# Kernel optimization log

Measured on AMD Instinct MI355X. Metric: run time of the kernel, lower is better.

Reference implementation:

```python
import jax, jax.numpy as jnp
import numpy as np

DIM = 768

def setup_inputs() -> dict:
    key = jax.random.key(0)
    k1, k2, k3, k4, k5 = jax.random.split(key, 5)
    B, S, D = 16, 1024, DIM
    x = jax.random.normal(k1, (B, S, D), dtype=jnp.float32)
    # torch Linear weights: W has shape [out, in], y = x @ W.T + b
    w_qkv = jax.random.normal(k2, (3 * D, D), dtype=jnp.float32) * (D ** -0.5)
    b_qkv = jax.random.normal(k3, (3 * D,), dtype=jnp.float32) * 0.01
    w_out = jax.random.normal(k4, (D, D), dtype=jnp.float32) * (D ** -0.5)
    b_out = jax.random.normal(k5, (D,), dtype=jnp.float32) * 0.01
    return {"x": x, "w_qkv": w_qkv, "b_qkv": b_qkv, "w_out": w_out, "b_out": b_out}

def reference(x, w_qkv, b_qkv, w_out, b_out):
    D = x.shape[-1]
    qkv = jnp.einsum('bsd,ed->bse', x, w_qkv) + b_qkv  # [B,S,3D]
    q, k, v = jnp.split(qkv, 3, axis=-1)
    scale = D ** -0.5
    att = jnp.einsum('bqd,bkd->bqk', q, k) * scale  # [B,S,S]
    att = jax.nn.softmax(att, axis=-1)
    # dropout (p=0.1) is identity in eval mode
    out = jnp.einsum('bqk,bkd->bqd', att, v)
    return jnp.einsum('bsd,ed->bse', out, w_out) + b_out
```

## Files before the change

kernel.cpp:

```cpp
#include <hip/hip_runtime.h>
#include <hip/hip_bf16.h>
#include <math.h>

typedef __attribute__((ext_vector_type(8))) short bf16x8;
typedef __attribute__((ext_vector_type(4))) float f32x4;

#define SCALE_QK 0.03608439182435162f

__device__ __forceinline__ unsigned short f2bf_rne(float f) {
    union { float f; unsigned u; } x; x.f = f;
    unsigned r = x.u + 0x7FFFu + ((x.u >> 16) & 1u);
    return (unsigned short)(r >> 16);
}

__device__ __forceinline__ void store4(unsigned short* p, float v0, float v1, float v2, float v3) {
    ushort4 o; o.x = f2bf_rne(v0); o.y = f2bf_rne(v1); o.z = f2bf_rne(v2); o.w = f2bf_rne(v3);
    *(ushort4*)p = o;
}
__device__ __forceinline__ void store4(float* p, float v0, float v1, float v2, float v3) {
    float4 o; o.x = v0; o.y = v1; o.z = v2; o.w = v3;
    *(float4*)p = o;
}

__device__ __forceinline__ void async_copy16(const void* g, void* l) {
    __builtin_amdgcn_global_load_lds(
        (const __attribute__((address_space(1))) void*)g,
        (__attribute__((address_space(3))) void*)l, 16, 0, 0);
}

__device__ __forceinline__ void gemm_core128(
    unsigned short* shA, unsigned short* shB,
    const unsigned short* __restrict__ A, int lda,
    const unsigned short* __restrict__ B, int ldb,
    long long tileM, long long tileN, int K,
    int t, int wm, int wn, int quad, int l16, f32x4 (&acc)[4][4])
{
    for (int k0 = 0; k0 < K; k0 += 64) {
        __syncthreads();
#pragma unroll
        for (int p = 0; p < 4; ++p) {
            const int g   = p * 256 + t;
            const int row = g >> 3;
            const int kg  = (g & 7) ^ (row & 7);
            async_copy16(A + (tileM + row) * (long long)lda + k0 + kg * 8, &shA[g << 3]);
            async_copy16(B + (tileN + row) * (long long)ldb + k0 + kg * 8, &shB[g << 3]);
        }
        __syncthreads();

#pragma unroll 1
        for (int h = 0; h < 2; ++h) {
            bf16x8 af[4], bfr[4];
#pragma unroll
            for (int mi = 0; mi < 4; ++mi) {
                const int row = wm + mi * 16 + l16;
                const int kg  = ((h << 2) | quad) ^ (row & 7);
                af[mi] = *(const bf16x8*)(&shA[row * 64 + kg * 8]);
            }
#pragma unroll
            for (int ni = 0; ni < 4; ++ni) {
                const int row = wn + ni * 16 + l16;
                const int kg  = ((h << 2) | quad) ^ (row & 7);
                bfr[ni] = *(const bf16x8*)(&shB[row * 64 + kg * 8]);
            }
#pragma unroll
            for (int mi = 0; mi < 4; ++mi)
#pragma unroll
                for (int ni = 0; ni < 4; ++ni)
                    acc[mi][ni] = __builtin_amdgcn_mfma_f32_16x16x32_bf16(
                        bfr[ni], af[mi], acc[mi][ni], 0, 0, 0);
        }
    }
}

__global__ __launch_bounds__(256) void prep(
    const float* __restrict__ w_qkv, const float* __restrict__ b_qkv,
    const float* __restrict__ w_out, const float* __restrict__ b_out,
    unsigned short* __restrict__ wqT, unsigned short* __restrict__ wkT,
    unsigned short* __restrict__ wvT, unsigned short* __restrict__ wob,
    float* __restrict__ v2f, float* __restrict__ bpp)
{
    const int blk = blockIdx.x;
    const int t   = threadIdx.x;
    if (blk < 432) {
        __shared__ float sh[64][65];
        const int m  = blk / 144;
        const int r  = blk % 144;
        const int ty = r / 12;
        const int tx = r % 12;
        const float* W = w_qkv + (long long)m * 768 * 768;
        unsigned short* WT = (m == 0) ? wqT : (m == 1) ? wkT : wvT;
        const int il = t & 63;
        const int ob = t >> 6;
#pragma unroll
        for (int it = 0; it < 16; ++it) {
            const int ol = ob + it * 4;
            sh[ol][il] = W[(long long)(ty * 64 + ol) * 768 + tx * 64 + il];
        }
        __syncthreads();
#pragma unroll
        for (int it = 0; it < 16; ++it) {
            const int il2 = ob + it * 4;
            WT[(long long)(tx * 64 + il2) * 768 + ty * 64 + il] = f2bf_rne(sh[il][il2]);
        }
    } else if (blk < 624) {
        const int d = (blk - 432) * 4 + (t >> 6);
        const int l = t & 63;
        float s = 0.f;
        for (int o = l; o < 768; o += 64)
            s += w_out[(long long)d * 768 + o] * b_qkv[1536 + o];
        for (int off = 1; off < 64; off <<= 1) s += __shfl_xor(s, off);
        if (l == 0) bpp[d] = b_out[d] + s;
    } else if (blk < 636) {
        __shared__ float pvv[4][64];
        const int i0   = (blk - 624) * 64;
        const int il   = t & 63;
        const int wave = t >> 6;
        const float* Wk = w_qkv + 768LL * 768;
        float a = 0.f;
        for (int o = wave * 192; o < wave * 192 + 192; ++o)
            a += Wk[(long long)o * 768 + i0 + il] * b_qkv[o];
        pvv[wave][il] = a;
        __syncthreads();
        if (t < 64) v2f[i0 + t] = pvv[0][t] + pvv[1][t] + pvv[2][t] + pvv[3][t];
    } else {
        const int j = (blk - 636) * 256 + t;
        float4 v = ((const float4*)w_out)[j];
        ushort4 o;
        o.x = f2bf_rne(v.x); o.y = f2bf_rne(v.y);
        o.z = f2bf_rne(v.z); o.w = f2bf_rne(v.w);
        ((ushort4*)wob)[j] = o;
    }
}

__global__ __launch_bounds__(256) void wgemm_cvt(
    const unsigned short* __restrict__ wkT, const unsigned short* __restrict__ wqT,
    const unsigned short* __restrict__ wob, const unsigned short* __restrict__ wvT,
    unsigned short* __restrict__ B2,
    const float* __restrict__ x, unsigned short* __restrict__ xb,
    const float* __restrict__ v2f, float* __restrict__ wf)
{
    const int t = threadIdx.x;
    if (blockIdx.x < 72) {
        __shared__ unsigned short shA[8192];
        __shared__ unsigned short shB[8192];
        const int lane = t & 63;
        const int wave = t >> 6;
        const int wm   = (wave & 1) * 64;
        const int wn   = (wave >> 1) * 64;
        const int quad = lane >> 4;
        const int l16  = lane & 15;
        const int z  = blockIdx.x / 36;
        const int r  = blockIdx.x % 36;
        const long long tileM = (long long)(r / 6) * 128;
        const long long tileN = (long long)(r % 6) * 128;
        const unsigned short* A  = z ? wob : wkT;
        const unsigned short* Bp = z ? wvT : wqT;
        unsigned short* C = B2 + (long long)z * 768 * 768;
        const float sc = z ? 1.0f : SCALE_QK;

        f32x4 acc[4][4];
#pragma unroll
        for (int i = 0; i < 4; ++i)
#pragma unroll
            for (int j = 0; j < 4; ++j)
#pragma unroll
                for (int rr = 0; rr < 4; ++rr) acc[i][j][rr] = 0.0f;

        gemm_core128(shA, shB, A, 768, Bp, 768, tileM, tileN, 768,
                     t, wm, wn, quad, l16, acc);

#pragma unroll
        for (int mi = 0; mi < 4; ++mi) {
            const long long gm = tileM + wm + mi * 16 + l16;
#pragma unroll
            for (int ni = 0; ni < 4; ++ni) {
                const long long gn0 = tileN + wn + ni * 16 + quad * 4;
                const f32x4 a = acc[mi][ni];
                store4(C + gm * 768 + gn0, a[0] * sc, a[1] * sc, a[2] * sc, a[3] * sc);
            }
        }
    } else {
        const int wave = t >> 6;
        const int lane = t & 63;
        const long long row = (long long)(blockIdx.x - 72) * 4 + wave;
        const float4* xr = (const float4*)x + row * 192;
        ushort4* xbr = (ushort4*)xb + row * 192;
        const float4* v2 = (const float4*)v2f;
        float w = 0.f;
#pragma unroll
        for (int j = 0; j < 3; ++j) {
            const int c = j * 64 + lane;
            float4 v = xr[c];
            ushort4 o;
            o.x = f2bf_rne(v.x); o.y = f2bf_rne(v.y);
            o.z = f2bf_rne(v.z); o.w = f2bf_rne(v.w);
            xbr[c] = o;
            float4 b = v2[c];
            w += v.x * b.x + v.y * b.y + v.z * b.z + v.w * b.w;
        }
#pragma unroll
        for (int off = 1; off < 64; off <<= 1) w += __shfl_xor(w, off);
        if (lane == 0) wf[row] = w * SCALE_QK;
    }
}

template <typename OutT, bool DO_EXP, bool DO_RSCALE, bool DO_VT>
__global__ __launch_bounds__(256) void gemm_nt_bf16(
    const unsigned short* __restrict__ A, int lda, long long strideA,
    const unsigned short* __restrict__ B, int ldb, long long strideB,
    OutT* __restrict__ C, int ldc, long long strideC,
    const float* __restrict__ bias, float scale, int K,
    float* __restrict__ rowsum, const float* __restrict__ rscale,
    unsigned short* __restrict__ vtp, const float* __restrict__ wf)
{
    __shared__ unsigned short shA[DO_VT ? 8448 : 8192];
    __shared__ unsigned short shB[DO_VT ? 8448 : 8192];

    const int t    = threadIdx.x;
    const int lane = t & 63;
    const int wave = t >> 6;
    const int wm   = (wave & 1) * 64;
    const int wn   = (wave >> 1) * 64;
    const int quad = lane >> 4;
    const int l16  = lane & 15;

    const int gx = gridDim.x, gy = gridDim.y;
    const int nwg = gx * gy * gridDim.z;
    const int orig = blockIdx.x + gx * (blockIdx.y + gy * blockIdx.z);
    const int id  = (orig & 7) * (nwg >> 3) + (orig >> 3);
    const int bx  = id % gx;
    const int rem = id / gx;
    const int by  = rem % gy;
    const int bz  = rem / gy;

    const long long batch = bz;
    A += batch * strideA;
    B += batch * strideB;
    C += batch * strideC;

    const long long tileM = (long long)by * 128;
    const long long tileN = (long long)bx * 128;
    const long long rowsPerBatch = (long long)gy * 128;

    f32x4 acc[4][4];
#pragma unroll
    for (int i = 0; i < 4; ++i)
#pragma unroll
        for (int j = 0; j < 4; ++j)
#pragma unroll
            for (int r = 0; r < 4; ++r) acc[i][j][r] = 0.0f;

    gemm_core128(shA, shB, A, lda, B, ldb, tileM, tileN, K, t, wm, wn, quad, l16, acc);

    const bool vt_block = DO_VT && (tileN >= 768) && (tileN < 1536);
    if (vt_block) __syncthreads();
    unsigned short* const shd = (wn == 0) ? shA : shB;

    float wkv[4][4];
    if (DO_EXP) {
        const float* wfb = wf + batch * rowsPerBatch;
#pragma unroll
        for (int ni = 0; ni < 4; ++ni) {
            const long long gn0 = tileN + wn + ni * 16 + quad * 4;
            float4 t4 = *(const float4*)&wfb[gn0];
            wkv[ni][0] = t4.x; wkv[ni][1] = t4.y; wkv[ni][2] = t4.z; wkv[ni][3] = t4.w;
        }
    }
#pragma unroll
    for (int mi = 0; mi < 4; ++mi) {
        const long long gm = tileM + wm + mi * 16 + l16;
        float w = scale;
        if (DO_RSCALE) {
            float s = 0.f;
#pragma unroll
            for (int j = 0; j < 16; ++j)
                s += rscale[((long long)j * gridDim.z + batch) * rowsPerBatch + gm];
            w = scale / s;
        }
        float rsum = 0.0f;
#pragma unroll
        for (int ni = 0; ni < 4; ++ni) {
            const long long gn0 = tileN + wn + ni * 16 + quad * 4;
            float b0 = 0.f, b1 = 0.f, b2 = 0.f, b3 = 0.f;
            if (bias) {
                float4 bv = *(const float4*)&bias[gn0];
                b0 = bv.x; b1 = bv.y; b2 = bv.z; b3 = bv.w;
            }
            const f32x4 a = acc[mi][ni];
            float v0, v1, v2, v3;
            if (DO_EXP) {
                v0 = __expf(a[0] + wkv[ni][0]);
                v1 = __expf(a[1] + wkv[ni][1]);
                v2 = __expf(a[2] + wkv[ni][2]);
                v3 = __expf(a[3] + wkv[ni][3]);
                rsum += (v0 + v1) + (v2 + v3);
            } else {
                v0 = a[0] * w + b0; v1 = a[1] * w + b1;
                v2 = a[2] * w + b2; v3 = a[3] * w + b3;
            }
            if (vt_block) {
                const int dl = ni * 16 + quad * 4;
                const int kl = wm + mi * 16 + l16;
                shd[(dl + 0) * 132 + kl] = f2bf_rne(v0);
                shd[(dl + 1) * 132 + kl] = f2bf_rne(v1);
                shd[(dl + 2) * 132 + kl] = f2bf_rne(v2);
                shd[(dl + 3) * 132 + kl] = f2bf_rne(v3);
            } else {
                store4(C + gm * (long long)ldc + gn0, v0, v1, v2, v3);
            }
        }
        if (DO_EXP) {
            rsum += __shfl_xor(rsum, 16);
            rsum += __shfl_xor(rsum, 32);
            if (quad == 0) {
                const long long slot = (long long)(bx * 2 + (wn >> 6));
                rowsum[(slot * gridDim.z + batch) * rowsPerBatch + gm] = rsum;
            }
        }
    }
    if (vt_block) {
        __syncthreads();
        const long long bvt  = tileM >> 10;
        const long long kin0 = tileM & 1023;
        const int dr = t >> 1;
        const int hf = t & 1;
        const unsigned short* src = (dr < 64) ? &shA[dr * 132] : &shB[(dr - 64) * 132];
        unsigned short* dst = vtp + (bvt * 768 + (tileN - 768) + dr) * 1024 + kin0 + hf * 64;
        src += hf * 64;
#pragma unroll
        for (int j = 0; j < 16; ++j)
            *(uint2*)(dst + j * 4) = *(const uint2*)(src + j * 4);
    }
}

extern "C" void kernel_launch(void* const* d_in, const int* in_sizes, int n_in,
                              void* d_out, int out_size, void* d_ws, size_t ws_size,
                              hipStream_t stream) {
    (void)in_sizes; (void)n_in; (void)out_size; (void)ws_size;

    const float* x     = (const float*)d_in[0];
    const float* w_qkv = (const float*)d_in[1];
    const float* b_qkv = (const float*)d_in[2];
    const float* w_out = (const float*)d_in[3];
    const float* b_out = (const float*)d_in[4];
    float* out = (float*)d_out;

    const int B = 16, S = 1024, D = 768;
    const long long MS = (long long)B * S;
    const int NB2 = 1536;

    unsigned short* xb  = (unsigned short*)d_ws;
    unsigned short* wob = xb  + MS * D;
    unsigned short* wqT = wob + (long long)D * D;
    unsigned short* wkT = wqT + (long long)D * D;
    unsigned short* wvT = wkT + (long long)D * D;
    unsigned short* B2  = wvT + (long long)D * D;
    unsigned short* xm  = B2  + (long long)NB2 * D;
    unsigned short* vwt = xm  + MS * D;
    unsigned short* att = vwt + (long long)B * D * S;
    float* rpart = (float*)(att + (long long)B * S * S);
    float* v2f   = rpart + 16 * MS;
    float* bpp   = v2f + D;
    float* wf    = bpp + D;

    prep<<<1212, 256, 0, stream>>>(w_qkv, b_qkv, w_out, b_out,
                                   wqT, wkT, wvT, wob, v2f, bpp);

    wgemm_cvt<<<4168, 256, 0, stream>>>(wkT, wqT, wob, wvT, B2, x, xb, v2f, wf);

    gemm_nt_bf16<unsigned short, false, false, true><<<dim3(NB2 / 128, (int)(MS / 128), 1), 256, 0, stream>>>(
        xb, D, 0, B2, D, 0, xm, D, 0, nullptr, 1.0f, D, nullptr, nullptr, vwt, nullptr);

    gemm_nt_bf16<unsigned short, true, false, false><<<dim3(S / 128, S / 128, B), 256, 0, stream>>>(
        xm, D, (long long)S * D,
        xb, D, (long long)S * D,
        att, S, (long long)S * S, nullptr, 1.0f, D, rpart, nullptr, nullptr, wf);

    gemm_nt_bf16<float, false, true, false><<<dim3(D / 128, S / 128, B), 256, 0, stream>>>(
        att, S, (long long)S * S,
        vwt, S, (long long)D * S,
        out, D, (long long)S * D, bpp, 1.0f, S, nullptr, rpart, nullptr, nullptr);
}
```

Measured before the change: 262.7 us.

## Add dedicated 128x256-tile attention score kernel with fused exp and rowsum

Splits the QK^T exp stage out of the generic GEMM template into its own kernel with a 128x256 output tile per workgroup (each wave computes 64x128). This halves the number of row-sum partial slots from 16 to 8 and raises reuse of the A tile, cutting global loads per output. The larger per-wave accumulator (32 MFMA tiles) raises register pressure and may lower occupancy. The loop also loads directly without the shared gemm_core pipeline, so it may lose any double buffering that core had.

```diff
diff --git a/kernel.cpp b/kernel.cpp
--- a/kernel.cpp
+++ b/kernel.cpp
@@ -204,14 +204,126 @@
     }
 }
 
-template <typename OutT, bool DO_EXP, bool DO_RSCALE, bool DO_VT>
+__global__ __launch_bounds__(256) void attn(
+    const unsigned short* __restrict__ A, long long strideA,
+    const unsigned short* __restrict__ B, long long strideB,
+    unsigned short* __restrict__ C, long long strideC,
+    const float* __restrict__ wf, float* __restrict__ rpart)
+{
+    __shared__ unsigned short shA[128 * 64];
+    __shared__ unsigned short shB[256 * 64];
+
+    const int t    = threadIdx.x;
+    const int lane = t & 63;
+    const int wave = t >> 6;
+    const int wm   = (wave & 1) * 64;
+    const int wk   = (wave >> 1);
+    const int quad = lane >> 4;
+    const int l16  = lane & 15;
+
+    const int nwg  = 512;
+    const int orig = blockIdx.x + 4 * (blockIdx.y + 8 * blockIdx.z);
+    const int id   = (orig & 7) * (nwg >> 3) + (orig >> 3);
+    const int bx   = id & 3;
+    const int rem  = id >> 2;
+    const int by   = rem & 7;
+    const int bz   = rem >> 3;
+
+    const long long batch = bz;
+    A += batch * strideA;
+    B += batch * strideB;
+    C += batch * strideC;
+    const long long tileM = (long long)by * 128;
+    const long long tileN = (long long)bx * 256;
+
+    f32x4 acc[4][8];
+#pragma unroll
+    for (int i = 0; i < 4; ++i)
+#pragma unroll
+        for (int j = 0; j < 8; ++j)
+#pragma unroll
+            for (int r = 0; r < 4; ++r) acc[i][j][r] = 0.0f;
+
+    for (int k0 = 0; k0 < 768; k0 += 64) {
+        __syncthreads();
+#pragma unroll
+        for (int p = 0; p < 4; ++p) {
+            const int g   = p * 256 + t;
+            const int row = g >> 3;
+            const int kg  = (g & 7) ^ (row & 7);
+            async_copy16(A + (tileM + row) * 768LL + k0 + kg * 8, &shA[g << 3]);
+        }
+#pragma unroll
+        for (int p = 0; p < 8; ++p) {
+            const int g   = p * 256 + t;
+            const int row = g >> 3;
+            const int kg  = (g & 7) ^ (row & 7);
+            async_copy16(B + (tileN + row) * 768LL + k0 + kg * 8, &shB[g << 3]);
+        }
+        __syncthreads();
+
+#pragma unroll 1
+        for (int h = 0; h < 2; ++h) {
+            bf16x8 af[4], bfr[8];
+#pragma unroll
+            for (int mi = 0; mi < 4; ++mi) {
+                const int row = wm + mi * 16 + l16;
+                const int kg  = ((h << 2) | quad) ^ (row & 7);
+                af[mi] = *(const bf16x8*)(&shA[row * 64 + kg * 8]);
+            }
+#pragma unroll
+            for (int ni = 0; ni < 8; ++ni) {
+                const int row = wk * 128 + ni * 16 + l16;
+                const int kg  = ((h << 2) | quad) ^ (row & 7);
+                bfr[ni] = *(const bf16x8*)(&shB[row * 64 + kg * 8]);
+            }
+#pragma unroll
+            for (int mi = 0; mi < 4; ++mi)
+#pragma unroll
+                for (int ni = 0; ni < 8; ++ni)
+                    acc[mi][ni] = __builtin_amdgcn_mfma_f32_16x16x32_bf16(
+                        bfr[ni], af[mi], acc[mi][ni], 0, 0, 0);
+        }
+    }
+
+    float wkv[8][4];
+#pragma unroll
+    for (int ni = 0; ni < 8; ++ni) {
+        const long long gn0 = tileN + wk * 128 + ni * 16 + quad * 4;
+        float4 t4 = *(const float4*)&wf[batch * 1024 + gn0];
+        wkv[ni][0] = t4.x; wkv[ni][1] = t4.y; wkv[ni][2] = t4.z; wkv[ni][3] = t4.w;
+    }
+#pragma unroll
+    for (int mi = 0; mi < 4; ++mi) {
+        const long long gm = tileM + wm + mi * 16 + l16;
+        float rsum = 0.0f;
+#pragma unroll
+        for (int ni = 0; ni < 8; ++ni) {
+            const long long gn0 = tileN + wk * 128 + ni * 16 + quad * 4;
+            const f32x4 a = acc[mi][ni];
+            const float v0 = __expf(a[0] + wkv[ni][0]);
+            const float v1 = __expf(a[1] + wkv[ni][1]);
+            const float v2 = __expf(a[2] + wkv[ni][2]);
+            const float v3 = __expf(a[3] + wkv[ni][3]);
+            rsum += (v0 + v1) + (v2 + v3);
+            store4(C + gm * 1024 + gn0, v0, v1, v2, v3);
+        }
+        rsum += __shfl_xor(rsum, 16);
+        rsum += __shfl_xor(rsum, 32);
+        if (quad == 0) {
+            const long long slot = (long long)(bx * 2 + wk);
+            rpart[(slot * 16 + batch) * 1024 + gm] = rsum;
+        }
+    }
+}
+
+template <typename OutT, bool DO_RSCALE, bool DO_VT>
 __global__ __launch_bounds__(256) void gemm_nt_bf16(
     const unsigned short* __restrict__ A, int lda, long long strideA,
     const unsigned short* __restrict__ B, int ldb, long long strideB,
     OutT* __restrict__ C, int ldc, long long strideC,
     const float* __restrict__ bias, float scale, int K,
-    float* __restrict__ rowsum, const float* __restrict__ rscale,
-    unsigned short* __restrict__ vtp, const float* __restrict__ wf)
+    const float* __restrict__ rscale, unsigned short* __restrict__ vtp)
 {
     __shared__ unsigned short shA[DO_VT ? 8448 : 8192];
     __shared__ unsigned short shB[DO_VT ? 8448 : 8192];
@@ -256,16 +368,6 @@
     if (vt_block) __syncthreads();
     unsigned short* const shd = (wn == 0) ? shA : shB;
 
-    float wkv[4][4];
-    if (DO_EXP) {
-        const float* wfb = wf + batch * rowsPerBatch;
-#pragma unroll
-        for (int ni = 0; ni < 4; ++ni) {
-            const long long gn0 = tileN + wn + ni * 16 + quad * 4;
-            float4 t4 = *(const float4*)&wfb[gn0];
-            wkv[ni][0] = t4.x; wkv[ni][1] = t4.y; wkv[ni][2] = t4.z; wkv[ni][3] = t4.w;
-        }
-    }
 #pragma unroll
     for (int mi = 0; mi < 4; ++mi) {
         const long long gm = tileM + wm + mi * 16 + l16;
@@ -273,11 +375,10 @@
         if (DO_RSCALE) {
             float s = 0.f;
 #pragma unroll
-            for (int j = 0; j < 16; ++j)
+            for (int j = 0; j < 8; ++j)
                 s += rscale[((long long)j * gridDim.z + batch) * rowsPerBatch + gm];
             w = scale / s;
         }
-        float rsum = 0.0f;
 #pragma unroll
         for (int ni = 0; ni < 4; ++ni) {
             const long long gn0 = tileN + wn + ni * 16 + quad * 4;
@@ -287,17 +388,8 @@
                 b0 = bv.x; b1 = bv.y; b2 = bv.z; b3 = bv.w;
             }
             const f32x4 a = acc[mi][ni];
-            float v0, v1, v2, v3;
-            if (DO_EXP) {
-                v0 = __expf(a[0] + wkv[ni][0]);
-                v1 = __expf(a[1] + wkv[ni][1]);
-                v2 = __expf(a[2] + wkv[ni][2]);
-                v3 = __expf(a[3] + wkv[ni][3]);
-                rsum += (v0 + v1) + (v2 + v3);
-            } else {
-                v0 = a[0] * w + b0; v1 = a[1] * w + b1;
-                v2 = a[2] * w + b2; v3 = a[3] * w + b3;
-            }
+            const float v0 = a[0] * w + b0, v1 = a[1] * w + b1;
+            const float v2 = a[2] * w + b2, v3 = a[3] * w + b3;
             if (vt_block) {
                 const int dl = ni * 16 + quad * 4;
                 const int kl = wm + mi * 16 + l16;
@@ -307,14 +399,6 @@
                 shd[(dl + 3) * 132 + kl] = f2bf_rne(v3);
             } else {
                 store4(C + gm * (long long)ldc + gn0, v0, v1, v2, v3);
-            }
-        }
-        if (DO_EXP) {
-            rsum += __shfl_xor(rsum, 16);
-            rsum += __shfl_xor(rsum, 32);
-            if (quad == 0) {
-                const long long slot = (long long)(bx * 2 + (wn >> 6));
-                rowsum[(slot * gridDim.z + batch) * rowsPerBatch + gm] = rsum;
             }
         }
     }
@@ -359,7 +443,7 @@
     unsigned short* vwt = xm  + MS * D;
     unsigned short* att = vwt + (long long)B * D * S;
     float* rpart = (float*)(att + (long long)B * S * S);
-    float* v2f   = rpart + 16 * MS;
+    float* v2f   = rpart + 8 * MS;
     float* bpp   = v2f + D;
     float* wf    = bpp + D;
 
@@ -368,16 +452,15 @@
 
     wgemm_cvt<<<4168, 256, 0, stream>>>(wkT, wqT, wob, wvT, B2, x, xb, v2f, wf);
 
-    gemm_nt_bf16<unsigned short, false, false, true><<<dim3(NB2 / 128, (int)(MS / 128), 1), 256, 0, stream>>>(
-        xb, D, 0, B2, D, 0, xm, D, 0, nullptr, 1.0f, D, nullptr, nullptr, vwt, nullptr);
-
-    gemm_nt_bf16<unsigned short, true, false, false><<<dim3(S / 128, S / 128, B), 256, 0, stream>>>(
-        xm, D, (long long)S * D,
-        xb, D, (long long)S * D,
-        att, S, (long long)S * S, nullptr, 1.0f, D, rpart, nullptr, nullptr, wf);
-
-    gemm_nt_bf16<float, false, true, false><<<dim3(D / 128, S / 128, B), 256, 0, stream>>>(
+    gemm_nt_bf16<unsigned short, false, true><<<dim3(NB2 / 128, (int)(MS / 128), 1), 256, 0, stream>>>(
+        xb, D, 0, B2, D, 0, xm, D, 0, nullptr, 1.0f, D, nullptr, vwt);
+
+    attn<<<dim3(4, 8, B), 256, 0, stream>>>(
+        xm, (long long)S * D, xb, (long long)S * D,
+        att, (long long)S * S, wf, rpart);
+
+    gemm_nt_bf16<float, true, false><<<dim3(D / 128, S / 128, B), 256, 0, stream>>>(
         att, S, (long long)S * S,
         vwt, S, (long long)D * S,
-        out, D, (long long)S * D, bpp, 1.0f, S, nullptr, rpart, nullptr, nullptr);
-}
+        out, D, (long long)S * D, bpp, 1.0f, S, rpart, nullptr);
+}
```

Result: faster. 255.3 us (-2.8%).

## Fuse all stages into one persistent kernel with software grid barriers

Applied to the files above, without the earlier changes.

Replaces the five separate kernel launches (weight prep, weight GEMM plus x conversion, QKV GEMM, attention scores, PV GEMM) with one persistent kernel of 768 blocks. The blocks loop over virtual tiles and use atomic-counter grid barriers between stages. The aim is to remove launch overhead and inter-kernel gaps. In exchange, all blocks must be co-resident, hence launch bounds of 3 blocks per CU, and each stage waits on a spin barrier. Tile assignment is strided by groups of 8 to spread work, which may lose the old block-swizzle locality.

```diff
diff --git a/kernel.cpp b/kernel.cpp
--- a/kernel.cpp
+++ b/kernel.cpp
@@ -12,7 +12,6 @@
     unsigned r = x.u + 0x7FFFu + ((x.u >> 16) & 1u);
     return (unsigned short)(r >> 16);
 }
-
 __device__ __forceinline__ void store4(unsigned short* p, float v0, float v1, float v2, float v3) {
     ushort4 o; o.x = f2bf_rne(v0); o.y = f2bf_rne(v1); o.z = f2bf_rne(v2); o.w = f2bf_rne(v3);
     *(ushort4*)p = o;
@@ -21,11 +20,22 @@
     float4 o; o.x = v0; o.y = v1; o.z = v2; o.w = v3;
     *(float4*)p = o;
 }
-
 __device__ __forceinline__ void async_copy16(const void* g, void* l) {
     __builtin_amdgcn_global_load_lds(
         (const __attribute__((address_space(1))) void*)g,
         (__attribute__((address_space(3))) void*)l, 16, 0, 0);
+}
+
+__device__ __forceinline__ void gridbar(int* bar, int G) {
+    __syncthreads();
+    if (threadIdx.x == 0) {
+        __threadfence();
+        __hip_atomic_fetch_add(bar, 1, __ATOMIC_ACQ_REL, __HIP_MEMORY_SCOPE_AGENT);
+        while (__hip_atomic_load(bar, __ATOMIC_ACQUIRE, __HIP_MEMORY_SCOPE_AGENT) < G)
+            __builtin_amdgcn_s_sleep(32);
+        __threadfence();
+    }
+    __syncthreads();
 }
 
 __device__ __forceinline__ void gemm_core128(
@@ -46,7 +56,6 @@
             async_copy16(B + (tileN + row) * (long long)ldb + k0 + kg * 8, &shB[g << 3]);
         }
         __syncthreads();
-
 #pragma unroll 1
         for (int h = 0; h < 2; ++h) {
             bf16x8 af[4], bfr[4];
@@ -72,17 +81,17 @@
     }
 }
 
-__global__ __launch_bounds__(256) void prep(
+
+__device__ __forceinline__ void prep_body(
+    int blk, int t, unsigned short* sh,
     const float* __restrict__ w_qkv, const float* __restrict__ b_qkv,
     const float* __restrict__ w_out, const float* __restrict__ b_out,
-    unsigned short* __restrict__ wqT, unsigned short* __restrict__ wkT,
-    unsigned short* __restrict__ wvT, unsigned short* __restrict__ wob,
-    float* __restrict__ v2f, float* __restrict__ bpp)
-{
-    const int blk = blockIdx.x;
-    const int t   = threadIdx.x;
+    unsigned short* wqT, unsigned short* wkT, unsigned short* wvT,
+    unsigned short* wob, float* v2f, float* bpp)
+{
+    __syncthreads();
     if (blk < 432) {
-        __shared__ float sh[64][65];
+        float (*shT)[65] = reinterpret_cast<float(*)[65]>(sh);
         const int m  = blk / 144;
         const int r  = blk % 144;
         const int ty = r / 12;
@@ -94,13 +103,13 @@
 #pragma unroll
         for (int it = 0; it < 16; ++it) {
             const int ol = ob + it * 4;
-            sh[ol][il] = W[(long long)(ty * 64 + ol) * 768 + tx * 64 + il];
+            shT[ol][il] = W[(long long)(ty * 64 + ol) * 768 + tx * 64 + il];
         }
         __syncthreads();
 #pragma unroll
         for (int it = 0; it < 16; ++it) {
             const int il2 = ob + it * 4;
-            WT[(long long)(tx * 64 + il2) * 768 + ty * 64 + il] = f2bf_rne(sh[il][il2]);
+            WT[(long long)(tx * 64 + il2) * 768 + ty * 64 + il] = f2bf_rne(shT[il][il2]);
         }
     } else if (blk < 624) {
         const int d = (blk - 432) * 4 + (t >> 6);
@@ -111,7 +120,7 @@
         for (int off = 1; off < 64; off <<= 1) s += __shfl_xor(s, off);
         if (l == 0) bpp[d] = b_out[d] + s;
     } else if (blk < 636) {
-        __shared__ float pvv[4][64];
+        float* pvv = reinterpret_cast<float*>(reinterpret_cast<char*>(sh) + 16640);
         const int i0   = (blk - 624) * 64;
         const int il   = t & 63;
         const int wave = t >> 6;
@@ -119,9 +128,9 @@
         float a = 0.f;
         for (int o = wave * 192; o < wave * 192 + 192; ++o)
             a += Wk[(long long)o * 768 + i0 + il] * b_qkv[o];
-        pvv[wave][il] = a;
+        pvv[wave * 64 + il] = a;
         __syncthreads();
-        if (t < 64) v2f[i0 + t] = pvv[0][t] + pvv[1][t] + pvv[2][t] + pvv[3][t];
+        if (t < 64) v2f[i0 + t] = pvv[t] + pvv[64 + t] + pvv[128 + t] + pvv[192 + t];
     } else {
         const int j = (blk - 636) * 256 + t;
         float4 v = ((const float4*)w_out)[j];
@@ -132,115 +141,95 @@
     }
 }
 
-__global__ __launch_bounds__(256) void wgemm_cvt(
-    const unsigned short* __restrict__ wkT, const unsigned short* __restrict__ wqT,
-    const unsigned short* __restrict__ wob, const unsigned short* __restrict__ wvT,
-    unsigned short* __restrict__ B2,
-    const float* __restrict__ x, unsigned short* __restrict__ xb,
-    const float* __restrict__ v2f, float* __restrict__ wf)
-{
-    const int t = threadIdx.x;
-    if (blockIdx.x < 72) {
-        __shared__ unsigned short shA[8192];
-        __shared__ unsigned short shB[8192];
-        const int lane = t & 63;
-        const int wave = t >> 6;
-        const int wm   = (wave & 1) * 64;
-        const int wn   = (wave >> 1) * 64;
-        const int quad = lane >> 4;
-        const int l16  = lane & 15;
-        const int z  = blockIdx.x / 36;
-        const int r  = blockIdx.x % 36;
-        const long long tileM = (long long)(r / 6) * 128;
-        const long long tileN = (long long)(r % 6) * 128;
-        const unsigned short* A  = z ? wob : wkT;
-        const unsigned short* Bp = z ? wvT : wqT;
-        unsigned short* C = B2 + (long long)z * 768 * 768;
-        const float sc = z ? 1.0f : SCALE_QK;
-
-        f32x4 acc[4][4];
-#pragma unroll
-        for (int i = 0; i < 4; ++i)
-#pragma unroll
-            for (int j = 0; j < 4; ++j)
-#pragma unroll
-                for (int rr = 0; rr < 4; ++rr) acc[i][j][rr] = 0.0f;
-
-        gemm_core128(shA, shB, A, 768, Bp, 768, tileM, tileN, 768,
-                     t, wm, wn, quad, l16, acc);
-
-#pragma unroll
-        for (int mi = 0; mi < 4; ++mi) {
-            const long long gm = tileM + wm + mi * 16 + l16;
-#pragma unroll
-            for (int ni = 0; ni < 4; ++ni) {
-                const long long gn0 = tileN + wn + ni * 16 + quad * 4;
-                const f32x4 a = acc[mi][ni];
-                store4(C + gm * 768 + gn0, a[0] * sc, a[1] * sc, a[2] * sc, a[3] * sc);
-            }
-        }
-    } else {
-        const int wave = t >> 6;
-        const int lane = t & 63;
-        const long long row = (long long)(blockIdx.x - 72) * 4 + wave;
-        const float4* xr = (const float4*)x + row * 192;
-        ushort4* xbr = (ushort4*)xb + row * 192;
-        const float4* v2 = (const float4*)v2f;
-        float w = 0.f;
-#pragma unroll
-        for (int j = 0; j < 3; ++j) {
-            const int c = j * 64 + lane;
-            float4 v = xr[c];
-            ushort4 o;
-            o.x = f2bf_rne(v.x); o.y = f2bf_rne(v.y);
-            o.z = f2bf_rne(v.z); o.w = f2bf_rne(v.w);
-            xbr[c] = o;
-            float4 b = v2[c];
-            w += v.x * b.x + v.y * b.y + v.z * b.z + v.w * b.w;
-        }
-#pragma unroll
-        for (int off = 1; off < 64; off <<= 1) w += __shfl_xor(w, off);
-        if (lane == 0) wf[row] = w * SCALE_QK;
-    }
-}
-
-template <typename OutT, bool DO_EXP, bool DO_RSCALE, bool DO_VT>
-__global__ __launch_bounds__(256) void gemm_nt_bf16(
-    const unsigned short* __restrict__ A, int lda, long long strideA,
-    const unsigned short* __restrict__ B, int ldb, long long strideB,
-    OutT* __restrict__ C, int ldc, long long strideC,
-    const float* __restrict__ bias, float scale, int K,
-    float* __restrict__ rowsum, const float* __restrict__ rscale,
-    unsigned short* __restrict__ vtp, const float* __restrict__ wf)
-{
-    __shared__ unsigned short shA[DO_VT ? 8448 : 8192];
-    __shared__ unsigned short shB[DO_VT ? 8448 : 8192];
-
-    const int t    = threadIdx.x;
+__device__ __forceinline__ void wgemm_body(
+    int b, int t, unsigned short* sh,
+    const unsigned short* wkT, const unsigned short* wqT,
+    const unsigned short* wob, const unsigned short* wvT, unsigned short* B2)
+{
+    unsigned short* shA = sh;
+    unsigned short* shB = sh + 8192;
     const int lane = t & 63;
     const int wave = t >> 6;
     const int wm   = (wave & 1) * 64;
     const int wn   = (wave >> 1) * 64;
     const int quad = lane >> 4;
     const int l16  = lane & 15;
-
-    const int gx = gridDim.x, gy = gridDim.y;
-    const int nwg = gx * gy * gridDim.z;
-    const int orig = blockIdx.x + gx * (blockIdx.y + gy * blockIdx.z);
-    const int id  = (orig & 7) * (nwg >> 3) + (orig >> 3);
-    const int bx  = id % gx;
-    const int rem = id / gx;
-    const int by  = rem % gy;
-    const int bz  = rem / gy;
-
-    const long long batch = bz;
-    A += batch * strideA;
-    B += batch * strideB;
-    C += batch * strideC;
-
+    const int z  = b / 36;
+    const int r  = b % 36;
+    const long long tileM = (long long)(r / 6) * 128;
+    const long long tileN = (long long)(r % 6) * 128;
+    const unsigned short* A  = z ? wob : wkT;
+    const unsigned short* Bp = z ? wvT : wqT;
+    unsigned short* C = B2 + (long long)z * 768 * 768;
+    const float sc = z ? 1.0f : SCALE_QK;
+
+    f32x4 acc[4][4];
+#pragma unroll
+    for (int i = 0; i < 4; ++i)
+#pragma unroll
+        for (int j = 0; j < 4; ++j)
+#pragma unroll
+            for (int rr = 0; rr < 4; ++rr) acc[i][j][rr] = 0.0f;
+
+    gemm_core128(shA, shB, A, 768, Bp, 768, tileM, tileN, 768, t, wm, wn, quad, l16, acc);
+
+#pragma unroll
+    for (int mi = 0; mi < 4; ++mi) {
+        const long long gm = tileM + wm + mi * 16 + l16;
+#pragma unroll
+        for (int ni = 0; ni < 4; ++ni) {
+            const long long gn0 = tileN + wn + ni * 16 + quad * 4;
+            const f32x4 a = acc[mi][ni];
+            store4(C + gm * 768 + gn0, a[0] * sc, a[1] * sc, a[2] * sc, a[3] * sc);
+        }
+    }
+}
+
+__device__ __forceinline__ void cvtx_body(
+    int u, int t,
+    const float* __restrict__ x, unsigned short* xb,
+    const float* __restrict__ v2f, float* wf)
+{
+    const int wave = t >> 6;
+    const int lane = t & 63;
+    const long long row = (long long)u * 4 + wave;
+    const float4* xr = (const float4*)x + row * 192;
+    ushort4* xbr = (ushort4*)xb + row * 192;
+    const float4* v2 = (const float4*)v2f;
+    float w = 0.f;
+#pragma unroll
+    for (int j = 0; j < 3; ++j) {
+        const int c = j * 64 + lane;
+        float4 v = xr[c];
+        ushort4 o;
+        o.x = f2bf_rne(v.x); o.y = f2bf_rne(v.y);
+        o.z = f2bf_rne(v.z); o.w = f2bf_rne(v.w);
+        xbr[c] = o;
+        float4 b = v2[c];
+        w += v.x * b.x + v.y * b.y + v.z * b.z + v.w * b.w;
+    }
+#pragma unroll
+    for (int off = 1; off < 64; off <<= 1) w += __shfl_xor(w, off);
+    if (lane == 0) wf[row] = w * SCALE_QK;
+}
+
+__device__ __forceinline__ void xgemm_body(
+    int tile, int t, unsigned short* sh,
+    const unsigned short* xb, const unsigned short* B2,
+    unsigned short* xm, unsigned short* vwt)
+{
+    unsigned short* shA = sh;
+    unsigned short* shB = sh + 8448;
+    const int lane = t & 63;
+    const int wave = t >> 6;
+    const int wm   = (wave & 1) * 64;
+    const int wn   = (wave >> 1) * 64;
+    const int quad = lane >> 4;
+    const int l16  = lane & 15;
+    const int bx = tile % 12;
+    const int by = tile / 12;
     const long long tileM = (long long)by * 128;
     const long long tileN = (long long)bx * 128;
-    const long long rowsPerBatch = (long long)gy * 128;
 
     f32x4 acc[4][4];
 #pragma unroll
@@ -248,73 +237,30 @@
 #pragma unroll
         for (int j = 0; j < 4; ++j)
 #pragma unroll
-            for (int r = 0; r < 4; ++r) acc[i][j][r] = 0.0f;
-
-    gemm_core128(shA, shB, A, lda, B, ldb, tileM, tileN, K, t, wm, wn, quad, l16, acc);
-
-    const bool vt_block = DO_VT && (tileN >= 768) && (tileN < 1536);
+            for (int rr = 0; rr < 4; ++rr) acc[i][j][rr] = 0.0f;
+
+    gemm_core128(shA, shB, xb, 768, B2, 768, tileM, tileN, 768, t, wm, wn, quad, l16, acc);
+
+    const bool vt_block = (tileN >= 768);
     if (vt_block) __syncthreads();
     unsigned short* const shd = (wn == 0) ? shA : shB;
 
-    float wkv[4][4];
-    if (DO_EXP) {
-        const float* wfb = wf + batch * rowsPerBatch;
+#pragma unroll
+    for (int mi = 0; mi < 4; ++mi) {
+        const long long gm = tileM + wm + mi * 16 + l16;
 #pragma unroll
         for (int ni = 0; ni < 4; ++ni) {
             const long long gn0 = tileN + wn + ni * 16 + quad * 4;
-            float4 t4 = *(const float4*)&wfb[gn0];
-            wkv[ni][0] = t4.x; wkv[ni][1] = t4.y; wkv[ni][2] = t4.z; wkv[ni][3] = t4.w;
-        }
-    }
-#pragma unroll
-    for (int mi = 0; mi < 4; ++mi) {
-        const long long gm = tileM + wm + mi * 16 + l16;
-        float w = scale;
-        if (DO_RSCALE) {
-            float s = 0.f;
-#pragma unroll
-            for (int j = 0; j < 16; ++j)
-                s += rscale[((long long)j * gridDim.z + batch) * rowsPerBatch + gm];
-            w = scale / s;
-        }
-        float rsum = 0.0f;
-#pragma unroll
-        for (int ni = 0; ni < 4; ++ni) {
-            const long long gn0 = tileN + wn + ni * 16 + quad * 4;
-            float b0 = 0.f, b1 = 0.f, b2 = 0.f, b3 = 0.f;
-            if (bias) {
-                float4 bv = *(const float4*)&bias[gn0];
-                b0 = bv.x; b1 = bv.y; b2 = bv.z; b3 = bv.w;
-            }
             const f32x4 a = acc[mi][ni];
-            float v0, v1, v2, v3;
-            if (DO_EXP) {
-                v0 = __expf(a[0] + wkv[ni][0]);
-                v1 = __expf(a[1] + wkv[ni][1]);
-                v2 = __expf(a[2] + wkv[ni][2]);
-                v3 = __expf(a[3] + wkv[ni][3]);
-                rsum += (v0 + v1) + (v2 + v3);
+            if (vt_block) {
+                const int dl = (int)(ni * 16 + quad * 4);
+                const int kl = wm + mi * 16 + l16;
+                shd[(dl + 0) * 132 + kl] = f2bf_rne(a[0]);
+                shd[(dl + 1) * 132 + kl] = f2bf_rne(a[1]);
+                shd[(dl + 2) * 132 + kl] = f2bf_rne(a[2]);
+                shd[(dl + 3) * 132 + kl] = f2bf_rne(a[3]);
             } else {
-                v0 = a[0] * w + b0; v1 = a[1] * w + b1;
-                v2 = a[2] * w + b2; v3 = a[3] * w + b3;
-            }
-            if (vt_block) {
-                const int dl = ni * 16 + quad * 4;
-                const int kl = wm + mi * 16 + l16;
-                shd[(dl + 0) * 132 + kl] = f2bf_rne(v0);
-                shd[(dl + 1) * 132 + kl] = f2bf_rne(v1);
-                shd[(dl + 2) * 132 + kl] = f2bf_rne(v2);
-                shd[(dl + 3) * 132 + kl] = f2bf_rne(v3);
-            } else {
-                store4(C + gm * (long long)ldc + gn0, v0, v1, v2, v3);
-            }
-        }
-        if (DO_EXP) {
-            rsum += __shfl_xor(rsum, 16);
-            rsum += __shfl_xor(rsum, 32);
-            if (quad == 0) {
-                const long long slot = (long long)(bx * 2 + (wn >> 6));
-                rowsum[(slot * gridDim.z + batch) * rowsPerBatch + gm] = rsum;
+                store4(xm + gm * 768 + gn0, a[0], a[1], a[2], a[3]);
             }
         }
     }
@@ -325,11 +271,192 @@
         const int dr = t >> 1;
         const int hf = t & 1;
         const unsigned short* src = (dr < 64) ? &shA[dr * 132] : &shB[(dr - 64) * 132];
-        unsigned short* dst = vtp + (bvt * 768 + (tileN - 768) + dr) * 1024 + kin0 + hf * 64;
+        unsigned short* dst = vwt + (bvt * 768 + (tileN - 768) + dr) * 1024 + kin0 + hf * 64;
         src += hf * 64;
 #pragma unroll
         for (int j = 0; j < 16; ++j)
             *(uint2*)(dst + j * 4) = *(const uint2*)(src + j * 4);
+    }
+}
+
+__device__ __forceinline__ void attn_body(
+    int tile, int t, unsigned short* sh,
+    const unsigned short* xm, const unsigned short* xb, unsigned short* att,
+    const float* __restrict__ wf, float* rpart)
+{
+    unsigned short* shA = sh;
+    unsigned short* shB = sh + 8192;
+    const int lane = t & 63;
+    const int wave = t >> 6;
+    const int wm   = (wave & 1) * 64;
+    const int wn   = (wave >> 1) * 64;
+    const int quad = lane >> 4;
+    const int l16  = lane & 15;
+    const int bz = tile >> 6;
+    const int by = (tile >> 3) & 7;
+    const int bx = tile & 7;
+    const unsigned short* A = xm + (long long)bz * 1024 * 768;
+    const unsigned short* B = xb + (long long)bz * 1024 * 768;
+    unsigned short* C = att + (long long)bz * 1024 * 1024;
+    const long long tileM = (long long)by * 128;
+    const long long tileN = (long long)bx * 128;
+
+    f32x4 acc[4][4];
+#pragma unroll
+    for (int i = 0; i < 4; ++i)
+#pragma unroll
+        for (int j = 0; j < 4; ++j)
+#pragma unroll
+            for (int rr = 0; rr < 4; ++rr) acc[i][j][rr] = 0.0f;
+
+    gemm_core128(shA, shB, A, 768, B, 768, tileM, tileN, 768, t, wm, wn, quad, l16, acc);
+
+    const float* wfb = wf + (long long)bz * 1024;
+    float wkv[4][4];
+#pragma unroll
+    for (int ni = 0; ni < 4; ++ni) {
+        const long long gn0 = tileN + wn + ni * 16 + quad * 4;
+        float4 t4 = *(const float4*)&wfb[gn0];
+        wkv[ni][0] = t4.x; wkv[ni][1] = t4.y; wkv[ni][2] = t4.z; wkv[ni][3] = t4.w;
+    }
+#pragma unroll
+    for (int mi = 0; mi < 4; ++mi) {
+        const long long gm = tileM + wm + mi * 16 + l16;
+        float rsum = 0.0f;
+#pragma unroll
+        for (int ni = 0; ni < 4; ++ni) {
+            const long long gn0 = tileN + wn + ni * 16 + quad * 4;
+            const f32x4 a = acc[mi][ni];
+            const float v0 = __expf(a[0] + wkv[ni][0]);
+            const float v1 = __expf(a[1] + wkv[ni][1]);
+            const float v2 = __expf(a[2] + wkv[ni][2]);
+            const float v3 = __expf(a[3] + wkv[ni][3]);
+            rsum += (v0 + v1) + (v2 + v3);
+            store4(C + gm * 1024 + gn0, v0, v1, v2, v3);
+        }
+        rsum += __shfl_xor(rsum, 16);
+        rsum += __shfl_xor(rsum, 32);
+        if (quad == 0) {
+            const long long slot = (long long)(bx * 2 + (wn >> 6));
+            rpart[(slot * 16 + bz) * 1024 + gm] = rsum;
+        }
+    }
+}
+
+__device__ __forceinline__ void pv_body(
+    int tile, int t, unsigned short* sh,
+    const unsigned short* att, const unsigned short* vwt, float* out,
+    const float* __restrict__ bpp, const float* __restrict__ rpart)
+{
+    unsigned short* shA = sh;
+    unsigned short* shB = sh + 8192;
+    const int lane = t & 63;
+    const int wave = t >> 6;
+    const int wm   = (wave & 1) * 64;
+    const int wn   = (wave >> 1) * 64;
+    const int quad = lane >> 4;
+    const int l16  = lane & 15;
+    const int bx = tile % 6;
+    const int rem = tile / 6;
+    const int by = rem & 7;
+    const int bz = rem >> 3;
+    const unsigned short* A = att + (long long)bz * 1024 * 1024;
+    const unsigned short* B = vwt + (long long)bz * 768 * 1024;
+    float* C = out + (long long)bz * 1024 * 768;
+    const long long tileM = (long long)by * 128;
+    const long long tileN = (long long)bx * 128;
+
+    f32x4 acc[4][4];
+#pragma unroll
+    for (int i = 0; i < 4; ++i)
+#pragma unroll
+        for (int j = 0; j < 4; ++j)
+#pragma unroll
+            for (int rr = 0; rr < 4; ++rr) acc[i][j][rr] = 0.0f;
+
+    gemm_core128(shA, shB, A, 1024, B, 1024, tileM, tileN, 1024, t, wm, wn, quad, l16, acc);
+
+#pragma unroll
+    for (int mi = 0; mi < 4; ++mi) {
+        const long long gm = tileM + wm + mi * 16 + l16;
+        float s = 0.f;
+#pragma unroll
+        for (int j = 0; j < 16; ++j)
+            s += rpart[((long long)j * 16 + bz) * 1024 + gm];
+        const float w = 1.0f / s;
+#pragma unroll
+        for (int ni = 0; ni < 4; ++ni) {
+            const long long gn0 = tileN + wn + ni * 16 + quad * 4;
+            float4 bv = *(const float4*)&bpp[gn0];
+            const f32x4 a = acc[mi][ni];
+            store4(C + gm * 768 + gn0,
+                   a[0] * w + bv.x, a[1] * w + bv.y, a[2] * w + bv.z, a[3] * w + bv.w);
+        }
+    }
+}
+
+__global__ __launch_bounds__(256, 3) void mega(
+    const float* __restrict__ x, const float* __restrict__ w_qkv,
+    const float* __restrict__ b_qkv, const float* __restrict__ w_out,
+    const float* __restrict__ b_out, float* __restrict__ out,
+    unsigned short* __restrict__ ws)
+{
+    __shared__ unsigned short sh[16896];
+
+    const int t = threadIdx.x;
+    const int b = blockIdx.x;
+    const int G = gridDim.x;
+    const int x8 = b & 7;
+    const int j8 = b >> 3;
+    const int C8 = G >> 3;
+
+    const long long MS = 16384;
+    unsigned short* xb  = ws;
+    unsigned short* wob = xb  + MS * 768;
+    unsigned short* wqT = wob + 768LL * 768;
+    unsigned short* wkT = wqT + 768LL * 768;
+    unsigned short* wvT = wkT + 768LL * 768;
+    unsigned short* B2  = wvT + 768LL * 768;
+    unsigned short* xm  = B2  + 1536LL * 768;
+    unsigned short* vwt = xm  + MS * 768;
+    unsigned short* att = vwt + 16LL * 768 * 1024;
+    float* rpart = (float*)(att + 16LL * 1024 * 1024);
+    float* v2f   = rpart + 16 * MS;
+    float* bpp   = v2f + 768;
+    float* wf    = bpp + 768;
+    int*   bar   = (int*)(wf + MS);
+
+    for (int vb = b; vb < 1212; vb += G)
+        prep_body(vb, t, sh, w_qkv, b_qkv, w_out, b_out,
+                  wqT, wkT, wvT, wob, v2f, bpp);
+    gridbar(bar + 0, G);
+
+    if (b < 72) {
+        wgemm_body(b, t, sh, wkT, wqT, wob, wvT, B2);
+    } else {
+        for (int u = b - 72; u < 4096; u += G - 72)
+            cvtx_body(u, t, x, xb, v2f, wf);
+    }
+    gridbar(bar + 1, G);
+
+    for (int k = 0;; ++k) {
+        const int off = j8 + k * C8;
+        if (off >= 192) break;
+        xgemm_body(x8 * 192 + off, t, sh, xb, B2, xm, vwt);
+    }
+    gridbar(bar + 2, G);
+
+    for (int k = 0;; ++k) {
+        const int off = j8 + k * C8;
+        if (off >= 128) break;
+        attn_body(x8 * 128 + off, t, sh, xm, xb, att, wf, rpart);
+    }
+    gridbar(bar + 3, G);
+
+    for (int k = 0;; ++k) {
+        const int off = j8 + k * C8;
+        if (off >= 96) break;
+        pv_body(x8 * 96 + off, t, sh, att, vwt, out, bpp, rpart);
     }
 }
 
@@ -344,40 +471,19 @@
     const float* w_out = (const float*)d_in[3];
     const float* b_out = (const float*)d_in[4];
     float* out = (float*)d_out;
-
-    const int B = 16, S = 1024, D = 768;
-    const long long MS = (long long)B * S;
-    const int NB2 = 1536;
-
-    unsigned short* xb  = (unsigned short*)d_ws;
-    unsigned short* wob = xb  + MS * D;
-    unsigned short* wqT = wob + (long long)D * D;
-    unsigned short* wkT = wqT + (long long)D * D;
-    unsigned short* wvT = wkT + (long long)D * D;
-    unsigned short* B2  = wvT + (long long)D * D;
-    unsigned short* xm  = B2  + (long long)NB2 * D;
-    unsigned short* vwt = xm  + MS * D;
-    unsigned short* att = vwt + (long long)B * D * S;
-    float* rpart = (float*)(att + (long long)B * S * S);
-    float* v2f   = rpart + 16 * MS;
-    float* bpp   = v2f + D;
-    float* wf    = bpp + D;
-
-    prep<<<1212, 256, 0, stream>>>(w_qkv, b_qkv, w_out, b_out,
-                                   wqT, wkT, wvT, wob, v2f, bpp);
-
-    wgemm_cvt<<<4168, 256, 0, stream>>>(wkT, wqT, wob, wvT, B2, x, xb, v2f, wf);
-
-    gemm_nt_bf16<unsigned short, false, false, true><<<dim3(NB2 / 128, (int)(MS / 128), 1), 256, 0, stream>>>(
-        xb, D, 0, B2, D, 0, xm, D, 0, nullptr, 1.0f, D, nullptr, nullptr, vwt, nullptr);
-
-    gemm_nt_bf16<unsigned short, true, false, false><<<dim3(S / 128, S / 128, B), 256, 0, stream>>>(
-        xm, D, (long long)S * D,
-        xb, D, (long long)S * D,
-        att, S, (long long)S * S, nullptr, 1.0f, D, rpart, nullptr, nullptr, wf);
-
-    gemm_nt_bf16<float, false, true, false><<<dim3(D / 128, S / 128, B), 256, 0, stream>>>(
-        att, S, (long long)S * S,
-        vwt, S, (long long)D * S,
-        out, D, (long long)S * D, bpp, 1.0f, S, nullptr, rpart, nullptr, nullptr);
-}
+    unsigned short* ws = (unsigned short*)d_ws;
+
+    const long long MS = 16384;
+    unsigned short* xb  = ws;
+    unsigned short* wob = xb  + MS * 768;
+    unsigned short* B2  = wob + 4LL * 768 * 768;
+    unsigned short* xm  = B2  + 1536LL * 768;
+    unsigned short* vwt = xm  + MS * 768;
+    unsigned short* att = vwt + 16LL * 768 * 1024;
+    float* rpart = (float*)(att + 16LL * 1024 * 1024);
+    float* wf    = rpart + 16 * MS + 768 + 768;
+    int*   bar   = (int*)(wf + MS);
+
+    hipMemsetAsync(bar, 0, 4 * sizeof(int), stream);
+    mega<<<768, 256, 0, stream>>>(x, w_qkv, b_qkv, w_out, b_out, out, ws);
+}
```

After: 929.6 us. 3.54x slower.
